# Kernel optimization log

Measured on AMD Instinct MI355X. Metric: run time of the kernel, lower is better.

The kernel has to match this reference:

```python
import jax, jax.numpy as jnp
import numpy as np

N, E = 50000, 800000
IN, H, OUT = 500, 128, 64


def _gcn_layer(x, src, dst, norm, W, b):
    # Linear transform first (PyG GCNConv applies lin before propagate)
    h = x @ W                                   # [N, F_out]
    msg = norm[:, None] * h[src]                # [E', F_out] gather
    out = jax.ops.segment_sum(msg, dst, num_segments=N)  # scatter-add
    return out + b


def setup_inputs() -> dict:
    key = jax.random.key(0)
    k = jax.random.split(key, 6)
    x = jax.random.normal(k[0], (N, IN), jnp.float32)
    edge_index = jax.random.randint(k[1], (2, E), 0, N, dtype=jnp.int32)
    # Glorot-style init like PyG GCNConv
    W1 = jax.random.normal(k[2], (IN, H), jnp.float32) * (1.0 / np.sqrt(IN))
    b1 = jnp.zeros((H,), jnp.float32)
    W2 = jax.random.normal(k[3], (H, OUT), jnp.float32) * (1.0 / np.sqrt(H))
    b2 = jnp.zeros((OUT,), jnp.float32)
    return {"x": x, "edge_index": edge_index, "W1": W1, "b1": b1, "W2": W2, "b2": b2}


def reference(x, edge_index, W1, b1, W2, b2):
    # Add self loops (PyG GCNConv default add_self_loops=True)
    loops = jnp.arange(N, dtype=edge_index.dtype)
    src = jnp.concatenate([edge_index[0], loops])
    dst = jnp.concatenate([edge_index[1], loops])
    # Symmetric degree normalization: deg computed on targets (col)
    deg = jax.ops.segment_sum(jnp.ones_like(src, dtype=x.dtype), dst, num_segments=N)
    dis = jnp.where(deg > 0, jax.lax.rsqrt(jnp.maximum(deg, 1.0)), 0.0)
    norm = dis[src] * dis[dst]                  # [E+N]
    h = jax.nn.relu(_gcn_layer(x, src, dst, norm, W1, b1))
    return _gcn_layer(h, src, dst, norm, W2, b2)
```

## Files before the change

kernel.cpp:

```cpp
#include <hip/hip_runtime.h>
#include <hip/hip_bf16.h>


typedef __attribute__((ext_vector_type(4))) float f32x4;
typedef __attribute__((ext_vector_type(8))) short short8;

static __device__ __forceinline__ unsigned short f2bf(float f) {
    unsigned int u = __float_as_uint(f);
    u += 0x7FFF + ((u >> 16) & 1);
    return (unsigned short)(u >> 16);
}
static __device__ __forceinline__ float bf2f(unsigned short h) {
    return __uint_as_float(((unsigned int)h) << 16);
}

static __device__ __forceinline__ void glds16(const void* g, void* l) {
    __builtin_amdgcn_global_load_lds(
        (const __attribute__((address_space(1))) void*)g,
        (__attribute__((address_space(3))) void*)l, 16, 0, 0);
}

__global__ void deg_accum_i(const int* __restrict__ dst, int* __restrict__ deg, int E) {
    int i = blockIdx.x * blockDim.x + threadIdx.x;
    if (i < E) atomicAdd(&deg[dst[i]], 1);
}

__global__ void prep_imgs(const float* __restrict__ W1, const float* __restrict__ W2,
                          unsigned short* __restrict__ I1, unsigned short* __restrict__ I2,
                          int* __restrict__ deg, int Nn) {
    int idx = blockIdx.x * 256 + threadIdx.x;
    if (idx < Nn) deg[idx] = 0;
    const int total1 = 16 * 1024;
    if (idx < total1) {
        int kt = idx >> 10, pl = (idx >> 9) & 1, slot = (idx >> 7) & 3, col = idx & 127;
        int k0 = kt * 32 + slot * 8;
#pragma unroll
        for (int j = 0; j < 8; j++) {
            int k = k0 + j;
            float v = (k < 500) ? W1[(size_t)k * 128 + col] : 0.f;
            unsigned short h = f2bf(v);
            I1[(size_t)idx * 8 + j] = pl ? f2bf(v - bf2f(h)) : h;
        }
    } else if (idx < total1 + 2048) {
        int i2 = idx - total1;
        int kt = i2 >> 9, pl = (i2 >> 8) & 1, slot = (i2 >> 6) & 3, col = i2 & 63;
        int k0 = kt * 32 + slot * 8;
#pragma unroll
        for (int j = 0; j < 8; j++) {
            float v = W2[(size_t)(k0 + j) * 64 + col];
            unsigned short h = f2bf(v);
            I2[(size_t)i2 * 8 + j] = pl ? f2bf(v - bf2f(h)) : h;
        }
    }
}

__global__ void scan_part(const int* __restrict__ deg, int* __restrict__ bsum, int N) {
    int tid = threadIdx.x, lane = tid & 63, wid = tid >> 6;
    int i = blockIdx.x * 256 + tid;
    int v = (i < N) ? deg[i] : 0;
#pragma unroll
    for (int off = 1; off < 64; off <<= 1) v += __shfl_xor(v, off, 64);
    __shared__ int ws[4];
    if (lane == 0) ws[wid] = v;
    __syncthreads();
    if (tid == 0) bsum[blockIdx.x] = ws[0] + ws[1] + ws[2] + ws[3];
}

__global__ __launch_bounds__(1024) void scan_top(const int* __restrict__ bsum, int nb,
                                                 int* __restrict__ boff, int* __restrict__ rp, int N) {
    __shared__ int wsum[16];
    int tid = threadIdx.x, lane = tid & 63, wid = tid >> 6;
    int v = (tid < nb) ? bsum[tid] : 0;
    int x = v;
#pragma unroll
    for (int off = 1; off < 64; off <<= 1) {
        int t = __shfl_up(x, off, 64);
        if (lane >= off) x += t;
    }
    if (lane == 63) wsum[wid] = x;
    __syncthreads();
    if (tid < 16) {
        int y = wsum[tid];
#pragma unroll
        for (int off = 1; off < 16; off <<= 1) {
            int t = __shfl_up(y, off, 16);
            if (tid >= off) y += t;
        }
        wsum[tid] = y;
    }
    __syncthreads();
    int base = wid ? wsum[wid - 1] : 0;
    if (tid < nb) boff[tid] = base + x - v;
    if (tid == 0) rp[N] = wsum[15];
}

__global__ void scan_final(int* __restrict__ deg, const int* __restrict__ boff,
                           int* __restrict__ rp, int* __restrict__ cursor, int N) {
    int tid = threadIdx.x, lane = tid & 63, wid = tid >> 6;
    int i = blockIdx.x * 256 + tid;
    int v = (i < N) ? deg[i] : 0;
    int x = v;
#pragma unroll
    for (int off = 1; off < 64; off <<= 1) {
        int t = __shfl_up(x, off, 64);
        if (lane >= off) x += t;
    }
    __shared__ int wsum[4];
    if (lane == 63) wsum[wid] = x;
    __syncthreads();
    int base = boff[blockIdx.x];
    for (int ww = 0; ww < wid; ww++) base += wsum[ww];
    int ex = base + x - v;
    if (i < N) {
        rp[i] = ex;
        cursor[i] = ex;
        ((float*)deg)[i] = rsqrtf((float)(v + 1));
    }
}

template<int BN, int KT, int KFULL>
__device__ __forceinline__ void gemm_body(
    int bid, unsigned char* sm,
    const float* __restrict__ A, const unsigned char* __restrict__ Wimg,
    unsigned short* __restrict__ C, int M, int K) {
    constexpr int ABYTES = 64 * 32 * 4;
    constexpr int BBYTES = BN * 128;
    constexpr int STEP = ABYTES + BBYTES;
    constexpr int AINST = ABYTES / 1024;
    constexpr int BINST = BBYTES / 1024;
    constexpr int IPW = (AINST + BINST) / 4;
    constexpr int BIPW = BINST / 4;
    constexpr int NF = BN / 16;

    const int tid = threadIdx.x, lane = tid & 63, w = tid >> 6;
    const int lrow = lane & 15, lq = lane >> 4;
    const int bm = bid * 64;

    f32x4 acc[NF] = {};

    float pr[8];
    if constexpr (KFULL < KT) {
        const int prow = tid >> 2, pk = (tid & 3) * 8;
        const int grow = bm + prow;
#pragma unroll
        for (int j = 0; j < 8; j++) {
            int k = KFULL * 32 + pk + j;
            pr[j] = (grow < M && k < K) ? A[(size_t)grow * K + k] : 0.f;
        }
    }

    auto STAGE = [&](int kt, int buf) {
        unsigned char* base = sm + buf * STEP;
#pragma unroll
        for (int j = 0; j < IPW; j++) {
            int g = w * IPW + j;
            if (g < AINST) {
                int srow = bm + lane; if (srow >= M) srow = M - 1;
                glds16(A + (size_t)srow * K + kt * 32 + g * 4, base + g * 1024);
            } else {
                int b = g - AINST;
                glds16(Wimg + (size_t)kt * BBYTES + (size_t)b * 1024 + lane * 16,
                       base + ABYTES + b * 1024);
            }
        }
    };
    auto STAGE_B = [&](int kt, int buf) {
        unsigned char* base = sm + buf * STEP;
#pragma unroll
        for (int j = 0; j < BIPW; j++) {
            int b = w * BIPW + j;
            glds16(Wimg + (size_t)kt * BBYTES + (size_t)b * 1024 + lane * 16,
                   base + ABYTES + b * 1024);
        }
    };
    auto REGWRITE = [&](int buf) {
        const int prow = tid >> 2, pk = (tid & 3) * 8;
        unsigned char* base = sm + buf * STEP;
        int s0 = pk >> 2;
        *(float4*)(base + s0 * 1024 + prow * 16) = make_float4(pr[0], pr[1], pr[2], pr[3]);
        *(float4*)(base + (s0 + 1) * 1024 + prow * 16) = make_float4(pr[4], pr[5], pr[6], pr[7]);
    };
    auto COMPUTE = [&](int buf) {
        const unsigned char* base = sm + buf * STEP;
        short8 ah, al;
        {
            int r = w * 16 + lrow;
            float4 f0 = *(const float4*)(base + (lq * 2) * 1024 + r * 16);
            float4 f1 = *(const float4*)(base + (lq * 2 + 1) * 1024 + r * 16);
            float fv[8] = {f0.x, f0.y, f0.z, f0.w, f1.x, f1.y, f1.z, f1.w};
#pragma unroll
            for (int e = 0; e < 8; e++) {
                unsigned short hu = f2bf(fv[e]);
                ah[e] = (short)hu;
                al[e] = (short)f2bf(fv[e] - bf2f(hu));
            }
        }
        short8 bh[NF], bl[NF];
#pragma unroll
        for (int n = 0; n < NF; n++) {
            int c = n * 16 + lrow;
            bh[n] = *(const short8*)(base + ABYTES + lq * (BN * 16) + c * 16);
            bl[n] = *(const short8*)(base + ABYTES + BBYTES / 2 + lq * (BN * 16) + c * 16);
        }
#pragma unroll
        for (int n = 0; n < NF; n++) {
            acc[n] = __builtin_amdgcn_mfma_f32_16x16x32_bf16(ah, bh[n], acc[n], 0, 0, 0);
            acc[n] = __builtin_amdgcn_mfma_f32_16x16x32_bf16(al, bh[n], acc[n], 0, 0, 0);
            acc[n] = __builtin_amdgcn_mfma_f32_16x16x32_bf16(ah, bl[n], acc[n], 0, 0, 0);
        }
    };

    STAGE(0, 0);
    __syncthreads();
    int cur = 0;
    for (int kt = 0; kt < KT; kt++) {
        if (kt + 1 < KT) {
            if constexpr (KFULL < KT) {
                if (kt + 1 == KFULL) { STAGE_B(kt + 1, cur ^ 1); REGWRITE(cur ^ 1); }
                else STAGE(kt + 1, cur ^ 1);
            } else {
                STAGE(kt + 1, cur ^ 1);
            }
        }
        COMPUTE(cur);
        __syncthreads();
        cur ^= 1;
    }

#pragma unroll
    for (int n = 0; n < NF; n++)
#pragma unroll
        for (int q = 0; q < 4; q++) {
            int row = bm + w * 16 + (lane >> 4) * 4 + q;
            int col = n * 16 + (lane & 15);
            if (row < M) C[(size_t)row * BN + col] = f2bf(acc[n][q]);
        }
}

template<int BN, int KT, int KFULL>
__global__ __launch_bounds__(256) void gemm_glds(
    const float* __restrict__ A, const unsigned char* __restrict__ Wimg,
    unsigned short* __restrict__ C, int M, int K) {
    __shared__ unsigned char sm[2 * (8192 + BN * 128)];
    gemm_body<BN, KT, KFULL>(blockIdx.x, sm, A, Wimg, C, M, K);
}

template<int BN, int KT, int KFULL>
__global__ __launch_bounds__(256) void fat_gemm_csr(
    const float* __restrict__ A, const unsigned char* __restrict__ Wimg,
    unsigned short* __restrict__ C, int M, int K,
    const int* __restrict__ src, const int* __restrict__ dst,
    int* __restrict__ cursor, int* __restrict__ csr_src, int E,
    int ngemm, int ncsr) {
    __shared__ unsigned char sm[2 * (8192 + BN * 128)];
    const int bid = blockIdx.x;
    const int stripe = bid / 5, pos = bid % 5;
    if (pos == 0) {
        if (stripe < ngemm)
            gemm_body<BN, KT, KFULL>(stripe, sm, A, Wimg, C, M, K);
    } else {
        int c = stripe * 4 + pos - 1;
        if (c < ncsr) {
            int e = c * 256 + threadIdx.x;
            if (e < E) {
                int p = atomicAdd(&cursor[dst[e]], 1);
                csr_src[p] = src[e];
            }
        }
    }
}

__global__ __launch_bounds__(256) void gather128(
    const int* __restrict__ rp, const int* __restrict__ csr,
    const float* __restrict__ dis, const unsigned short* __restrict__ h,
    const float* __restrict__ bias, float* __restrict__ out, int Nn) {
    int n = (blockIdx.x * 256 + threadIdx.x) >> 6;
    int lane = threadIdx.x & 63;
    if (n >= Nn) return;
    const int hh = lane >> 5;
    const int l = lane & 31;
    int beg = rp[n], end = rp[n + 1];
    float4 a0 = {0,0,0,0}, a1 = {0,0,0,0}, a2 = {0,0,0,0}, a3 = {0,0,0,0};
    auto P = [&](int e, float4& a) {
        int s = csr[e];
        float w = dis[s];
        ushort4 v = *(const ushort4*)&h[(size_t)s * 128 + l * 4];
        a.x = fmaf(w, bf2f(v.x), a.x); a.y = fmaf(w, bf2f(v.y), a.y);
        a.z = fmaf(w, bf2f(v.z), a.z); a.w = fmaf(w, bf2f(v.w), a.w);
    };
    int j = beg + hh;
    for (; j + 6 < end; j += 8) { P(j, a0); P(j + 2, a1); P(j + 4, a2); P(j + 6, a3); }
    for (; j < end; j += 2) P(j, a0);
    float4 acc;
    acc.x = (a0.x + a1.x) + (a2.x + a3.x);
    acc.y = (a0.y + a1.y) + (a2.y + a3.y);
    acc.z = (a0.z + a1.z) + (a2.z + a3.z);
    acc.w = (a0.w + a1.w) + (a2.w + a3.w);
    acc.x += __shfl_xor(acc.x, 32);
    acc.y += __shfl_xor(acc.y, 32);
    acc.z += __shfl_xor(acc.z, 32);
    acc.w += __shfl_xor(acc.w, 32);
    float dn = dis[n];
    ushort4 hv = *(const ushort4*)&h[(size_t)n * 128 + l * 4];
    float4 b4 = *(const float4*)&bias[l * 4];
    float4 o;
    o.x = fmaxf(dn * (acc.x + dn * bf2f(hv.x)) + b4.x, 0.f);
    o.y = fmaxf(dn * (acc.y + dn * bf2f(hv.y)) + b4.y, 0.f);
    o.z = fmaxf(dn * (acc.z + dn * bf2f(hv.z)) + b4.z, 0.f);
    o.w = fmaxf(dn * (acc.w + dn * bf2f(hv.w)) + b4.w, 0.f);
    if (hh == 0) *(float4*)&out[(size_t)n * 128 + l * 4] = o;
}

__global__ __launch_bounds__(256) void gather64(
    const int* __restrict__ rp, const int* __restrict__ csr,
    const float* __restrict__ dis, const unsigned short* __restrict__ h,
    const float* __restrict__ bias, float* __restrict__ out, int Nn) {
    int n = (blockIdx.x * 256 + threadIdx.x) >> 6;
    int lane = threadIdx.x & 63;
    if (n >= Nn) return;
    const int q = lane >> 4;
    const int l = lane & 15;
    int beg = rp[n], end = rp[n + 1];
    float4 a0 = {0,0,0,0}, a1 = {0,0,0,0};
    auto P = [&](int e, float4& a) {
        int s = csr[e];
        float w = dis[s];
        ushort4 v = *(const ushort4*)&h[(size_t)s * 64 + l * 4];
        a.x = fmaf(w, bf2f(v.x), a.x); a.y = fmaf(w, bf2f(v.y), a.y);
        a.z = fmaf(w, bf2f(v.z), a.z); a.w = fmaf(w, bf2f(v.w), a.w);
    };
    int j = beg + q;
    for (; j + 4 < end; j += 8) { P(j, a0); P(j + 4, a1); }
    for (; j < end; j += 4) P(j, a0);
    float4 acc;
    acc.x = a0.x + a1.x; acc.y = a0.y + a1.y;
    acc.z = a0.z + a1.z; acc.w = a0.w + a1.w;
    acc.x += __shfl_xor(acc.x, 16); acc.x += __shfl_xor(acc.x, 32);
    acc.y += __shfl_xor(acc.y, 16); acc.y += __shfl_xor(acc.y, 32);
    acc.z += __shfl_xor(acc.z, 16); acc.z += __shfl_xor(acc.z, 32);
    acc.w += __shfl_xor(acc.w, 16); acc.w += __shfl_xor(acc.w, 32);
    float dn = dis[n];
    ushort4 hv = *(const ushort4*)&h[(size_t)n * 64 + l * 4];
    float4 b4 = *(const float4*)&bias[l * 4];
    float4 o;
    o.x = dn * (acc.x + dn * bf2f(hv.x)) + b4.x;
    o.y = dn * (acc.y + dn * bf2f(hv.y)) + b4.y;
    o.z = dn * (acc.z + dn * bf2f(hv.z)) + b4.z;
    o.w = dn * (acc.w + dn * bf2f(hv.w)) + b4.w;
    if (q == 0) *(float4*)&out[(size_t)n * 64 + l * 4] = o;
}

extern "C" void kernel_launch(void* const* d_in, const int* in_sizes, int n_in,
                              void* d_out, int out_size, void* d_ws, size_t ws_size,
                              hipStream_t stream) {
    const float* x  = (const float*)d_in[0];
    const int*   ei = (const int*)d_in[1];
    const float* W1 = (const float*)d_in[2];
    const float* b1 = (const float*)d_in[3];
    const float* W2 = (const float*)d_in[4];
    const float* b2 = (const float*)d_in[5];

    const int IN = 500, H = 128, OUT = 64;
    const int Nn = in_sizes[0] / IN;
    const int E  = in_sizes[1] / 2;
    const int* src  = ei;
    const int* dstp = ei + E;

    const int Npad = ((Nn + 63) / 64) * 64;
    const int nb   = (Nn + 255) / 256;
    const int ngemm = (Nn + 63) / 64;
    const int ncsr  = (E + 255) / 256;

    int*   degdis  = (int*)d_ws;
    int*   rp      = degdis + Npad;
    int*   bsum    = rp + Npad + 64;
    int*   boff    = bsum + 1024;
    int*   cursor  = boff + 1024;
    int*   csr_src = cursor + Npad;
    unsigned short* I1 = (unsigned short*)(csr_src + ((E + 63) / 64) * 64);
    unsigned short* I2 = I1 + 16 * 8192;
    unsigned short* h1u = I2 + 4 * 4096;
    float* agg1    = (float*)(h1u + (size_t)Npad * H);
    unsigned short* h2u = h1u;
    float* dis     = (float*)degdis;
    float* out     = (float*)d_out;

    prep_imgs<<<(Nn + 255) / 256, 256, 0, stream>>>(W1, W2, I1, I2, degdis, Nn);
    deg_accum_i<<<ncsr, 256, 0, stream>>>(dstp, degdis, E);
    scan_part<<<nb, 256, 0, stream>>>(degdis, bsum, Nn);
    scan_top<<<1, 1024, 0, stream>>>(bsum, nb, boff, rp, Nn);
    scan_final<<<nb, 256, 0, stream>>>(degdis, boff, rp, cursor, Nn);

    fat_gemm_csr<128, 16, 15><<<ngemm * 5, 256, 0, stream>>>(
        x, (const unsigned char*)I1, h1u, Nn, IN,
        src, dstp, cursor, csr_src, E, ngemm, ncsr);

    gather128<<<(Nn + 3) / 4, 256, 0, stream>>>(rp, csr_src, dis, h1u, b1, agg1, Nn);

    gemm_glds<64, 4, 4><<<ngemm, 256, 0, stream>>>(
        agg1, (const unsigned char*)I2, h2u, Nn, H);
    gather64<<<(Nn + 3) / 4, 256, 0, stream>>>(rp, csr_src, dis, h2u, b2, out, Nn);
}
```

Baseline: 185.6 us.

## Fuse second-layer weight GEMM into layer-1 gather epilogue

Removes the separate MFMA GEMM for layer 2 and the fp32 agg1 intermediate. Each wave's aggregated, ReLU'd 128-wide row now goes to LDS and is multiplied by W2 with scalar FMAs, writing bf16 h2 directly. W2 is also no longer split into a bf16 hi/lo image. This saves one kernel launch and a full write and read of a 50000x128 fp32 buffer. In exchange the gather kernel does 128 FMAs per lane per node on plain fp32 ALUs and reads W2 from global or cache every time.

```diff
diff --git a/kernel.cpp b/kernel.cpp
--- a/kernel.cpp
+++ b/kernel.cpp
@@ -26,7 +26,7 @@
 }
 
 __global__ void prep_imgs(const float* __restrict__ W1, const float* __restrict__ W2,
-                          unsigned short* __restrict__ I1, unsigned short* __restrict__ I2,
+                          unsigned short* __restrict__ I1,
                           int* __restrict__ deg, int Nn) {
     int idx = blockIdx.x * 256 + threadIdx.x;
     if (idx < Nn) deg[idx] = 0;
@@ -40,16 +40,6 @@
             float v = (k < 500) ? W1[(size_t)k * 128 + col] : 0.f;
             unsigned short h = f2bf(v);
             I1[(size_t)idx * 8 + j] = pl ? f2bf(v - bf2f(h)) : h;
-        }
-    } else if (idx < total1 + 2048) {
-        int i2 = idx - total1;
-        int kt = i2 >> 9, pl = (i2 >> 8) & 1, slot = (i2 >> 6) & 3, col = i2 & 63;
-        int k0 = kt * 32 + slot * 8;
-#pragma unroll
-        for (int j = 0; j < 8; j++) {
-            float v = W2[(size_t)(k0 + j) * 64 + col];
-            unsigned short h = f2bf(v);
-            I2[(size_t)i2 * 8 + j] = pl ? f2bf(v - bf2f(h)) : h;
         }
     }
 }
@@ -235,14 +225,6 @@
             int col = n * 16 + (lane & 15);
             if (row < M) C[(size_t)row * BN + col] = f2bf(acc[n][q]);
         }
-}
-
-template<int BN, int KT, int KFULL>
-__global__ __launch_bounds__(256) void gemm_glds(
-    const float* __restrict__ A, const unsigned char* __restrict__ Wimg,
-    unsigned short* __restrict__ C, int M, int K) {
-    __shared__ unsigned char sm[2 * (8192 + BN * 128)];
-    gemm_body<BN, KT, KFULL>(blockIdx.x, sm, A, Wimg, C, M, K);
 }
 
 template<int BN, int KT, int KFULL>
@@ -270,23 +252,27 @@
     }
 }
 
-__global__ __launch_bounds__(256) void gather128(
+__global__ __launch_bounds__(256) void gather128_g2(
     const int* __restrict__ rp, const int* __restrict__ csr,
     const float* __restrict__ dis, const unsigned short* __restrict__ h,
-    const float* __restrict__ bias, float* __restrict__ out, int Nn) {
+    const float* __restrict__ bias, const float* __restrict__ W2,
+    unsigned short* __restrict__ h2, int Nn) {
+    __shared__ float rowbuf[4][128];
     int n = (blockIdx.x * 256 + threadIdx.x) >> 6;
     int lane = threadIdx.x & 63;
-    if (n >= Nn) return;
+    int w = threadIdx.x >> 6;
+    const bool valid = n < Nn;
+    const int nc = valid ? n : (Nn - 1);
     const int hh = lane >> 5;
     const int l = lane & 31;
-    int beg = rp[n], end = rp[n + 1];
+    int beg = rp[nc], end = rp[nc + 1];
     float4 a0 = {0,0,0,0}, a1 = {0,0,0,0}, a2 = {0,0,0,0}, a3 = {0,0,0,0};
     auto P = [&](int e, float4& a) {
         int s = csr[e];
-        float w = dis[s];
+        float ww = dis[s];
         ushort4 v = *(const ushort4*)&h[(size_t)s * 128 + l * 4];
-        a.x = fmaf(w, bf2f(v.x), a.x); a.y = fmaf(w, bf2f(v.y), a.y);
-        a.z = fmaf(w, bf2f(v.z), a.z); a.w = fmaf(w, bf2f(v.w), a.w);
+        a.x = fmaf(ww, bf2f(v.x), a.x); a.y = fmaf(ww, bf2f(v.y), a.y);
+        a.z = fmaf(ww, bf2f(v.z), a.z); a.w = fmaf(ww, bf2f(v.w), a.w);
     };
     int j = beg + hh;
     for (; j + 6 < end; j += 8) { P(j, a0); P(j + 2, a1); P(j + 4, a2); P(j + 6, a3); }
@@ -300,15 +286,27 @@
     acc.y += __shfl_xor(acc.y, 32);
     acc.z += __shfl_xor(acc.z, 32);
     acc.w += __shfl_xor(acc.w, 32);
-    float dn = dis[n];
-    ushort4 hv = *(const ushort4*)&h[(size_t)n * 128 + l * 4];
+    float dn = dis[nc];
+    ushort4 hv = *(const ushort4*)&h[(size_t)nc * 128 + l * 4];
     float4 b4 = *(const float4*)&bias[l * 4];
     float4 o;
     o.x = fmaxf(dn * (acc.x + dn * bf2f(hv.x)) + b4.x, 0.f);
     o.y = fmaxf(dn * (acc.y + dn * bf2f(hv.y)) + b4.y, 0.f);
     o.z = fmaxf(dn * (acc.z + dn * bf2f(hv.z)) + b4.z, 0.f);
     o.w = fmaxf(dn * (acc.w + dn * bf2f(hv.w)) + b4.w, 0.f);
-    if (hh == 0) *(float4*)&out[(size_t)n * 128 + l * 4] = o;
+    if (hh == 0) *(float4*)&rowbuf[w][l * 4] = o;
+    __syncthreads();
+    float c0 = 0.f, c1 = 0.f, c2 = 0.f, c3 = 0.f;
+#pragma unroll 4
+    for (int k = 0; k < 128; k += 4) {
+        float r0 = rowbuf[w][k], r1 = rowbuf[w][k + 1];
+        float r2 = rowbuf[w][k + 2], r3 = rowbuf[w][k + 3];
+        c0 = fmaf(r0, W2[(size_t)(k + 0) * 64 + lane], c0);
+        c1 = fmaf(r1, W2[(size_t)(k + 1) * 64 + lane], c1);
+        c2 = fmaf(r2, W2[(size_t)(k + 2) * 64 + lane], c2);
+        c3 = fmaf(r3, W2[(size_t)(k + 3) * 64 + lane], c3);
+    }
+    if (valid) h2[(size_t)n * 64 + lane] = f2bf((c0 + c1) + (c2 + c3));
 }
 
 __global__ __launch_bounds__(256) void gather64(
@@ -378,14 +376,12 @@
     int*   cursor  = boff + 1024;
     int*   csr_src = cursor + Npad;
     unsigned short* I1 = (unsigned short*)(csr_src + ((E + 63) / 64) * 64);
-    unsigned short* I2 = I1 + 16 * 8192;
-    unsigned short* h1u = I2 + 4 * 4096;
-    float* agg1    = (float*)(h1u + (size_t)Npad * H);
-    unsigned short* h2u = h1u;
+    unsigned short* h1u = I1 + 16 * 8192;
+    unsigned short* h2u = h1u + (size_t)Npad * H;
     float* dis     = (float*)degdis;
     float* out     = (float*)d_out;
 
-    prep_imgs<<<(Nn + 255) / 256, 256, 0, stream>>>(W1, W2, I1, I2, degdis, Nn);
+    prep_imgs<<<(Nn + 255) / 256, 256, 0, stream>>>(W1, W2, I1, degdis, Nn);
     deg_accum_i<<<ncsr, 256, 0, stream>>>(dstp, degdis, E);
     scan_part<<<nb, 256, 0, stream>>>(degdis, bsum, Nn);
     scan_top<<<1, 1024, 0, stream>>>(bsum, nb, boff, rp, Nn);
@@ -395,9 +391,7 @@
         x, (const unsigned char*)I1, h1u, Nn, IN,
         src, dstp, cursor, csr_src, E, ngemm, ncsr);
 
-    gather128<<<(Nn + 3) / 4, 256, 0, stream>>>(rp, csr_src, dis, h1u, b1, agg1, Nn);
-
-    gemm_glds<64, 4, 4><<<ngemm, 256, 0, stream>>>(
-        agg1, (const unsigned char*)I2, h2u, Nn, H);
+    gather128_g2<<<(Nn + 3) / 4, 256, 0, stream>>>(rp, csr_src, dis, h1u, b1, W2, h2u, Nn);
+
     gather64<<<(Nn + 3) / 4, 256, 0, stream>>>(rp, csr_src, dis, h2u, b2, out, Nn);
 }
```

After: 212.6 us. 1.15x slower.
